# Kernel tuning notes

Measured on AMD Instinct MI355X. Metric: run time of the kernel, lower is better.

Reference implementation:

```python
import jax, jax.numpy as jnp
import numpy as np

EPS = 1e-8  # torch F.cosine_similarity eps


def setup_inputs() -> dict:
    key = jax.random.key(0)
    B, CAP, CD, CTX = 32, 32768, 64, 64
    ks = jax.random.split(key, 9)
    inp = {
        "query_content": jax.random.normal(ks[0], (B, CD), jnp.float32),
        "query_context": jax.random.normal(ks[1], (B, CTX), jnp.float32),
        "memory_content": 0.1 * jax.random.normal(ks[2], (CAP, CD), jnp.float32),
        "memory_contexts": 0.1 * jax.random.normal(ks[3], (CAP, CTX), jnp.float32),
        "memory_freshness": jnp.ones((CAP,), jnp.float32),
        "W1": jax.random.normal(ks[4], (2 * CD, CD), jnp.float32) / np.sqrt(2 * CD),
        "b1": 0.01 * jax.random.normal(ks[5], (CD,), jnp.float32),
        "W2": jax.random.normal(ks[6], (CD, 1), jnp.float32) / np.sqrt(CD),
        "b2": 0.01 * jax.random.normal(ks[7], (1,), jnp.float32),
        "top_k": 16,
    }
    return inp


def reference(query_content, query_context, memory_content, memory_contexts,
              memory_freshness, W1, b1, W2, b2, top_k):
    B, CD = query_content.shape
    # similarity_calculator MLP over all (query, memory) pairs.
    # Linear on concat([q, m]) == q @ W1[:CD] + m @ W1[CD:]  (avoids the concat).
    q_part = query_content @ W1[:CD]            # [B, CD]
    m_part = memory_content @ W1[CD:]           # [CAP, CD]
    h = jax.nn.relu(q_part[:, None, :] + m_part[None, :, :] + b1)  # [B, CAP, CD]
    content_sim = jax.nn.sigmoid(jnp.einsum('bch,h->bc', h, W2[:, 0]) + b2[0])  # [B, CAP]

    # cosine similarity between query_context and each stored context
    qn = query_context / jnp.maximum(jnp.linalg.norm(query_context, axis=-1, keepdims=True), EPS)
    mn = memory_contexts / jnp.maximum(jnp.linalg.norm(memory_contexts, axis=-1, keepdims=True), EPS)
    context_sim = qn @ mn.T                      # [B, CAP]

    time_weights = memory_freshness              # time_mask is all-ones in source
    final = 0.5 * content_sim + 0.3 * context_sim + 0.2 * time_weights[None, :]

    top_similarities, top_indices = jax.lax.top_k(final, top_k)   # [B, k]
    retrieved_content = memory_content[top_indices]               # [B, k, CD]
    retrieved_time_weights = time_weights[top_indices]            # [B, k]
    return (retrieved_content, top_similarities, retrieved_time_weights)
```

## Files before the change

kernel.cpp:

```cpp
#include <hip/hip_runtime.h>
#include <math.h>

#define CAP   32768
#define NB    32
#define ROWS  64
#define NBLK  (CAP / ROWS)
#define TOPK  16
#define CEPS  1e-8f

#define PITCH 68
#define CHUNK 2048
#define NCHUNK (CAP / CHUNK)

#define WS_QP    0
#define WS_QN    2048
#define WS_FINAL 4096

__global__ __launch_bounds__(64) void prep_kernel(
    const float* __restrict__ qc,
    const float* __restrict__ qctx,
    const float* __restrict__ W1,
    const float* __restrict__ b1,
    float* __restrict__ ws)
{
    const int b = blockIdx.x;
    const int j = threadIdx.x;

    float a0 = b1[j], a1 = 0.f, a2 = 0.f, a3 = 0.f;
    #pragma unroll
    for (int i = 0; i < 64; i += 4) {
        a0 = fmaf(qc[b * 64 + i + 0], W1[(i + 0) * 64 + j], a0);
        a1 = fmaf(qc[b * 64 + i + 1], W1[(i + 1) * 64 + j], a1);
        a2 = fmaf(qc[b * 64 + i + 2], W1[(i + 2) * 64 + j], a2);
        a3 = fmaf(qc[b * 64 + i + 3], W1[(i + 3) * 64 + j], a3);
    }
    ws[WS_QP + b * 64 + j] = (a0 + a1) + (a2 + a3);

    float x = qctx[b * 64 + j];
    float ss = x * x;
    ss += __shfl_xor(ss, 1,  64);
    ss += __shfl_xor(ss, 2,  64);
    ss += __shfl_xor(ss, 4,  64);
    ss += __shfl_xor(ss, 8,  64);
    ss += __shfl_xor(ss, 16, 64);
    ss += __shfl_xor(ss, 32, 64);
    ws[WS_QN + b * 64 + j] = x / fmaxf(sqrtf(ss), CEPS);
}

__global__ __launch_bounds__(256) void score_kernel(
    const float* __restrict__ mcont,
    const float* __restrict__ mctx,
    const float* __restrict__ fresh,
    const float* __restrict__ W1,
    const float* __restrict__ W2,
    const float* __restrict__ b2,
    float* __restrict__ ws)
{
    __shared__ float s_mc[ROWS * PITCH];
    __shared__ float s_qp[NB * PITCH];
    __shared__ float s_qn[NB * PITCH];
    __shared__ float s_base[ROWS];
    __shared__ float s_inv[ROWS];

    const int tid = threadIdx.x;
    const int C0 = blockIdx.x * ROWS;

    const float4* g_mc = (const float4*)(mcont + (size_t)C0 * 64);
    #pragma unroll
    for (int t = tid; t < ROWS * 16; t += 256) {
        int r = t >> 4, c4 = t & 15;
        *(float4*)&s_mc[r * PITCH + c4 * 4] = g_mc[t];
    }
    const float4* g_qp = (const float4*)(ws + WS_QP);
    const float4* g_qn = (const float4*)(ws + WS_QN);
    #pragma unroll
    for (int t = tid; t < NB * 16; t += 256) {
        int r = t >> 4, c4 = t & 15;
        *(float4*)&s_qp[r * PITCH + c4 * 4] = g_qp[t];
        *(float4*)&s_qn[r * PITCH + c4 * 4] = g_qn[t];
    }
    {
        const int r = tid >> 2, q = tid & 3;
        const float* xr = mctx + (size_t)(C0 + r) * 64 + q * 16;
        float ss = 0.f;
        #pragma unroll
        for (int i = 0; i < 4; ++i) {
            float4 x = *(const float4*)&xr[i * 4];
            ss = fmaf(x.x, x.x, ss); ss = fmaf(x.y, x.y, ss);
            ss = fmaf(x.z, x.z, ss); ss = fmaf(x.w, x.w, ss);
        }
        ss += __shfl_xor(ss, 1, 64);
        ss += __shfl_xor(ss, 2, 64);
        if (q == 0) {
            s_inv[r]  = 0.3f / fmaxf(sqrtf(ss), CEPS);
            s_base[r] = 0.2f * fresh[C0 + r];
        }
    }
    __syncthreads();

    const int c_lo = tid & 15;
    const int j0 = (tid >> 4) * 4;
    {
        float acc[4][4] = {{0.f}};
        #pragma unroll 4
        for (int i4 = 0; i4 < 16; ++i4) {
            float4 w0 = *(const float4*)&W1[(64 + i4 * 4 + 0) * 64 + j0];
            float4 w1r = *(const float4*)&W1[(64 + i4 * 4 + 1) * 64 + j0];
            float4 w2r = *(const float4*)&W1[(64 + i4 * 4 + 2) * 64 + j0];
            float4 w3r = *(const float4*)&W1[(64 + i4 * 4 + 3) * 64 + j0];
            #pragma unroll
            for (int ci = 0; ci < 4; ++ci) {
                float4 m = *(const float4*)&s_mc[(c_lo + 16 * ci) * PITCH + i4 * 4];
                acc[ci][0] = fmaf(m.x, w0.x, acc[ci][0]);
                acc[ci][1] = fmaf(m.x, w0.y, acc[ci][1]);
                acc[ci][2] = fmaf(m.x, w0.z, acc[ci][2]);
                acc[ci][3] = fmaf(m.x, w0.w, acc[ci][3]);
                acc[ci][0] = fmaf(m.y, w1r.x, acc[ci][0]);
                acc[ci][1] = fmaf(m.y, w1r.y, acc[ci][1]);
                acc[ci][2] = fmaf(m.y, w1r.z, acc[ci][2]);
                acc[ci][3] = fmaf(m.y, w1r.w, acc[ci][3]);
                acc[ci][0] = fmaf(m.z, w2r.x, acc[ci][0]);
                acc[ci][1] = fmaf(m.z, w2r.y, acc[ci][1]);
                acc[ci][2] = fmaf(m.z, w2r.z, acc[ci][2]);
                acc[ci][3] = fmaf(m.z, w2r.w, acc[ci][3]);
                acc[ci][0] = fmaf(m.w, w3r.x, acc[ci][0]);
                acc[ci][1] = fmaf(m.w, w3r.y, acc[ci][1]);
                acc[ci][2] = fmaf(m.w, w3r.z, acc[ci][2]);
                acc[ci][3] = fmaf(m.w, w3r.w, acc[ci][3]);
            }
        }
        __syncthreads();
        #pragma unroll
        for (int jj = 0; jj < 4; ++jj)
            #pragma unroll
            for (int ci = 0; ci < 4; ++ci)
                s_mc[(j0 + jj) * PITCH + c_lo + 16 * ci] = acc[ci][jj];
    }
    __syncthreads();

    const int bq = (tid & 15) << 1;
    const int cq = (tid >> 4) << 2;
    float4 a1v[2];
    a1v[0] = make_float4(0.f, 0.f, 0.f, 0.f);
    a1v[1] = make_float4(0.f, 0.f, 0.f, 0.f);
    float a2[2][4] = {{0.f}};
    const float* mxb = mctx + (size_t)C0 * 64;

    #pragma unroll 4
    for (int j4 = 0; j4 < 16; ++j4) {
        const int jo = j4 * 4;
        float4 w2v = *(const float4*)(W2 + jo);
        float4 qp0 = *(const float4*)&s_qp[ bq      * PITCH + jo];
        float4 qp1 = *(const float4*)&s_qp[(bq + 1) * PITCH + jo];
        float4 qn0 = *(const float4*)&s_qn[ bq      * PITCH + jo];
        float4 qn1 = *(const float4*)&s_qn[(bq + 1) * PITCH + jo];
        float4 m0 = *(const float4*)&s_mc[(jo + 0) * PITCH + cq];
        float4 m1 = *(const float4*)&s_mc[(jo + 1) * PITCH + cq];
        float4 m2 = *(const float4*)&s_mc[(jo + 2) * PITCH + cq];
        float4 m3 = *(const float4*)&s_mc[(jo + 3) * PITCH + cq];

        #pragma unroll
        for (int bi = 0; bi < 2; ++bi) {
            float4 qp = bi ? qp1 : qp0;
            float4& av = a1v[bi];
            av.x = fmaf(fmaxf(qp.x + m0.x, 0.f), w2v.x, av.x);
            av.y = fmaf(fmaxf(qp.x + m0.y, 0.f), w2v.x, av.y);
            av.z = fmaf(fmaxf(qp.x + m0.z, 0.f), w2v.x, av.z);
            av.w = fmaf(fmaxf(qp.x + m0.w, 0.f), w2v.x, av.w);
            av.x = fmaf(fmaxf(qp.y + m1.x, 0.f), w2v.y, av.x);
            av.y = fmaf(fmaxf(qp.y + m1.y, 0.f), w2v.y, av.y);
            av.z = fmaf(fmaxf(qp.y + m1.z, 0.f), w2v.y, av.z);
            av.w = fmaf(fmaxf(qp.y + m1.w, 0.f), w2v.y, av.w);
            av.x = fmaf(fmaxf(qp.z + m2.x, 0.f), w2v.z, av.x);
            av.y = fmaf(fmaxf(qp.z + m2.y, 0.f), w2v.z, av.y);
            av.z = fmaf(fmaxf(qp.z + m2.z, 0.f), w2v.z, av.z);
            av.w = fmaf(fmaxf(qp.z + m2.w, 0.f), w2v.z, av.w);
            av.x = fmaf(fmaxf(qp.w + m3.x, 0.f), w2v.w, av.x);
            av.y = fmaf(fmaxf(qp.w + m3.y, 0.f), w2v.w, av.y);
            av.z = fmaf(fmaxf(qp.w + m3.z, 0.f), w2v.w, av.z);
            av.w = fmaf(fmaxf(qp.w + m3.w, 0.f), w2v.w, av.w);
        }
        #pragma unroll
        for (int ci = 0; ci < 4; ++ci) {
            float4 xv = *(const float4*)&mxb[(cq + ci) * 64 + jo];
            a2[0][ci] = fmaf(qn0.x, xv.x, a2[0][ci]);
            a2[0][ci] = fmaf(qn0.y, xv.y, a2[0][ci]);
            a2[0][ci] = fmaf(qn0.z, xv.z, a2[0][ci]);
            a2[0][ci] = fmaf(qn0.w, xv.w, a2[0][ci]);
            a2[1][ci] = fmaf(qn1.x, xv.x, a2[1][ci]);
            a2[1][ci] = fmaf(qn1.y, xv.y, a2[1][ci]);
            a2[1][ci] = fmaf(qn1.z, xv.z, a2[1][ci]);
            a2[1][ci] = fmaf(qn1.w, xv.w, a2[1][ci]);
        }
    }

    const float b2v = b2[0];
    float4 inv4  = *(const float4*)&s_inv[cq];
    float4 base4 = *(const float4*)&s_base[cq];
    #pragma unroll
    for (int bi = 0; bi < 2; ++bi) {
        float4 r;
        r.x = 0.5f / (1.f + expf(-(a1v[bi].x + b2v))) + a2[bi][0] * inv4.x + base4.x;
        r.y = 0.5f / (1.f + expf(-(a1v[bi].y + b2v))) + a2[bi][1] * inv4.y + base4.y;
        r.z = 0.5f / (1.f + expf(-(a1v[bi].z + b2v))) + a2[bi][2] * inv4.z + base4.z;
        r.w = 0.5f / (1.f + expf(-(a1v[bi].w + b2v))) + a2[bi][3] * inv4.w + base4.w;
        *(float4*)&ws[WS_FINAL + (size_t)(bq + bi) * CAP + C0 + cq] = r;
    }
}

__device__ __forceinline__ void bitonic64_desc(float& v, int& iv, int lane)
{
    #pragma unroll
    for (int k = 2; k <= 64; k <<= 1) {
        #pragma unroll
        for (int j = k >> 1; j > 0; j >>= 1) {
            float ov = __shfl_xor(v, j, 64);
            int   oi = __shfl_xor(iv, j, 64);
            bool low        = (lane & j) == 0;
            bool dirDesc    = (lane & k) == 0;
            bool takeBetter = (low == dirDesc);
            bool otherBetter = (ov > v) || (ov == v && oi < iv);
            if (otherBetter == takeBetter) { v = ov; iv = oi; }
        }
    }
}

__global__ __launch_bounds__(256) void topk_stage1(float* __restrict__ ws)
{
    __shared__ float s_val[64];
    __shared__ int   s_idx[64];

    const int lane = threadIdx.x & 63;
    const int w    = threadIdx.x >> 6;
    const int b    = blockIdx.y;
    float* row = ws + WS_FINAL + (size_t)b * CAP;
    const int cbase = blockIdx.x * CHUNK;
    const int sb = cbase + w * 512;

    float v[8];
    #pragma unroll
    for (int g = 0; g < 2; ++g) {
        float4 t = *(const float4*)&row[sb + g * 256 + lane * 4];
        v[4 * g + 0] = t.x; v[4 * g + 1] = t.y;
        v[4 * g + 2] = t.z; v[4 * g + 3] = t.w;
    }

    float outv = 0.f;
    int   outi = 0;

    for (int k = 0; k < TOPK; ++k) {
        float bv = v[0]; int bj = 0;
        #pragma unroll
        for (int j = 1; j < 8; ++j)
            if (v[j] > bv) { bv = v[j]; bj = j; }
        int bi = sb + (bj >> 2) * 256 + lane * 4 + (bj & 3);

        #pragma unroll
        for (int off = 1; off < 64; off <<= 1) {
            float ov = __shfl_xor(bv, off, 64);
            int   oi = __shfl_xor(bi, off, 64);
            if (ov > bv || (ov == bv && oi < bi)) { bv = ov; bi = oi; }
        }
        if (lane == k) { outv = bv; outi = bi; }

        int rel = bi - sb;
        bool mine = (((rel >> 2) & 63) == lane);
        int wj = ((rel >> 8) << 2) | (rel & 3);
        #pragma unroll
        for (int j = 0; j < 8; ++j)
            if (mine && wj == j) v[j] = -INFINITY;
    }

    if (lane < TOPK) {
        s_val[w * TOPK + lane] = outv;
        s_idx[w * TOPK + lane] = outi;
    }
    __syncthreads();
    if (w != 0) return;

    float mv = s_val[lane];
    int   mi = s_idx[lane];
    bitonic64_desc(mv, mi, lane);
    if (lane < TOPK) {
        row[cbase + lane]        = mv;
        row[cbase + TOPK + lane] = __int_as_float(mi);
    }
}

__global__ __launch_bounds__(256) void topk_stage2(
    const float* __restrict__ mcont,
    const float* __restrict__ fresh,
    const float* __restrict__ ws,
    float* __restrict__ out)
{
    __shared__ float s_val[64];
    __shared__ int   s_idx[64];

    const int lane = threadIdx.x & 63;
    const int w    = threadIdx.x >> 6;
    const int b    = blockIdx.x;
    const float* row = ws + WS_FINAL + (size_t)b * CAP;

    const int ch  = w * 4 + (lane >> 4);
    const int pos = lane & 15;
    float mv = row[ch * CHUNK + pos];
    int   mi = __float_as_int(row[ch * CHUNK + TOPK + pos]);
    bitonic64_desc(mv, mi, lane);

    if (lane < TOPK) {
        s_val[w * TOPK + lane] = mv;
        s_idx[w * TOPK + lane] = mi;
    }
    __syncthreads();
    if (w != 0) return;

    float fv = s_val[lane];
    int   fi = s_idx[lane];
    bitonic64_desc(fv, fi, lane);

    float* out_content = out;
    float* out_sim     = out + NB * TOPK * 64;
    float* out_tw      = out + NB * TOPK * 64 + NB * TOPK;

    if (lane < TOPK) {
        out_sim[b * TOPK + lane] = fv;
        out_tw [b * TOPK + lane] = fresh[fi];
    }

    #pragma unroll
    for (int r = 0; r < TOPK; ++r) {
        int wi = __shfl(fi, r, 64);
        out_content[(size_t)b * TOPK * 64 + r * 64 + lane] =
            mcont[(size_t)wi * 64 + lane];
    }
}

extern "C" void kernel_launch(void* const* d_in, const int* in_sizes, int n_in,
                              void* d_out, int out_size, void* d_ws, size_t ws_size,
                              hipStream_t stream) {
    const float* qc    = (const float*)d_in[0];
    const float* qctx  = (const float*)d_in[1];
    const float* mcont = (const float*)d_in[2];
    const float* mctx  = (const float*)d_in[3];
    const float* fresh = (const float*)d_in[4];
    const float* W1    = (const float*)d_in[5];
    const float* b1    = (const float*)d_in[6];
    const float* W2    = (const float*)d_in[7];
    const float* b2    = (const float*)d_in[8];
    float* out = (float*)d_out;
    float* ws  = (float*)d_ws;

    prep_kernel<<<NB, 64, 0, stream>>>(qc, qctx, W1, b1, ws);
    score_kernel<<<NBLK, 256, 0, stream>>>(mcont, mctx, fresh, W1, W2, b2, ws);
    topk_stage1<<<dim3(NCHUNK, NB), 256, 0, stream>>>(ws);
    topk_stage2<<<NB, 256, 0, stream>>>(mcont, fresh, ws, out);
}
```

Measured before the change: 125.9 us.

## Replace iterative top-k extraction with bitonic sorts and halve chunk size

Stage-1 top-k previously ran 16 rounds of wave-wide argmax reductions over 8 values per lane. It now sorts four 64-element columns with bitonic networks and merges their top-16s with one more bitonic pass. The chunk size drops to 1024, which doubles the number of stage-1 blocks. Stage 2 grows to 512 threads with an extra merge level to absorb the 32 chunk candidate lists. This trades serial shuffle reductions for parallel sorting networks, at the cost of more blocks and more intermediate candidates.

Measured after the change: 125.9 us, median of 2. About the same (-0.0%).

```diff
diff --git a/kernel.cpp b/kernel.cpp
--- a/kernel.cpp
+++ b/kernel.cpp
@@ -9,7 +9,7 @@
 #define CEPS  1e-8f
 
 #define PITCH 68
-#define CHUNK 2048
+#define CHUNK 1024
 #define NCHUNK (CAP / CHUNK)
 
 #define WS_QP    0
@@ -235,45 +235,34 @@
     const int b    = blockIdx.y;
     float* row = ws + WS_FINAL + (size_t)b * CAP;
     const int cbase = blockIdx.x * CHUNK;
-    const int sb = cbase + w * 512;
-
-    float v[8];
-    #pragma unroll
-    for (int g = 0; g < 2; ++g) {
-        float4 t = *(const float4*)&row[sb + g * 256 + lane * 4];
-        v[4 * g + 0] = t.x; v[4 * g + 1] = t.y;
-        v[4 * g + 2] = t.z; v[4 * g + 3] = t.w;
-    }
-
-    float outv = 0.f;
-    int   outi = 0;
-
-    for (int k = 0; k < TOPK; ++k) {
-        float bv = v[0]; int bj = 0;
-        #pragma unroll
-        for (int j = 1; j < 8; ++j)
-            if (v[j] > bv) { bv = v[j]; bj = j; }
-        int bi = sb + (bj >> 2) * 256 + lane * 4 + (bj & 3);
-
-        #pragma unroll
-        for (int off = 1; off < 64; off <<= 1) {
-            float ov = __shfl_xor(bv, off, 64);
-            int   oi = __shfl_xor(bi, off, 64);
-            if (ov > bv || (ov == bv && oi < bi)) { bv = ov; bi = oi; }
-        }
-        if (lane == k) { outv = bv; outi = bi; }
-
-        int rel = bi - sb;
-        bool mine = (((rel >> 2) & 63) == lane);
-        int wj = ((rel >> 8) << 2) | (rel & 3);
-        #pragma unroll
-        for (int j = 0; j < 8; ++j)
-            if (mine && wj == j) v[j] = -INFINITY;
-    }
+    const int sb = cbase + w * 256;
+
+    float4 t = *(const float4*)&row[sb + lane * 4];
+    float v0 = t.x, v1 = t.y, v2 = t.z, v3 = t.w;
+    int   i0 = sb + lane * 4 + 0;
+    int   i1 = sb + lane * 4 + 1;
+    int   i2 = sb + lane * 4 + 2;
+    int   i3 = sb + lane * 4 + 3;
+
+    bitonic64_desc(v0, i0, lane);
+    bitonic64_desc(v1, i1, lane);
+    bitonic64_desc(v2, i2, lane);
+    bitonic64_desc(v3, i3, lane);
+
+    const int r = lane & 15;
+    float c0 = __shfl(v0, r, 64), c1 = __shfl(v1, r, 64);
+    float c2 = __shfl(v2, r, 64), c3 = __shfl(v3, r, 64);
+    int   d0 = __shfl(i0, r, 64), d1 = __shfl(i1, r, 64);
+    int   d2 = __shfl(i2, r, 64), d3 = __shfl(i3, r, 64);
+    const int s = lane >> 4;
+    float cv = (s == 0) ? c0 : (s == 1) ? c1 : (s == 2) ? c2 : c3;
+    int   ci = (s == 0) ? d0 : (s == 1) ? d1 : (s == 2) ? d2 : d3;
+
+    bitonic64_desc(cv, ci, lane);
 
     if (lane < TOPK) {
-        s_val[w * TOPK + lane] = outv;
-        s_idx[w * TOPK + lane] = outi;
+        s_val[w * TOPK + lane] = cv;
+        s_idx[w * TOPK + lane] = ci;
     }
     __syncthreads();
     if (w != 0) return;
@@ -287,35 +276,49 @@
     }
 }
 
-__global__ __launch_bounds__(256) void topk_stage2(
+__global__ __launch_bounds__(512) void topk_stage2(
     const float* __restrict__ mcont,
     const float* __restrict__ fresh,
     const float* __restrict__ ws,
     float* __restrict__ out)
 {
-    __shared__ float s_val[64];
-    __shared__ int   s_idx[64];
+    __shared__ float s_v1[128];
+    __shared__ int   s_i1[128];
+    __shared__ float s_v2[32];
+    __shared__ int   s_i2[32];
 
     const int lane = threadIdx.x & 63;
     const int w    = threadIdx.x >> 6;
     const int b    = blockIdx.x;
     const float* row = ws + WS_FINAL + (size_t)b * CAP;
 
-    const int ch  = w * 4 + (lane >> 4);
-    const int pos = lane & 15;
-    float mv = row[ch * CHUNK + pos];
-    int   mi = __float_as_int(row[ch * CHUNK + TOPK + pos]);
-    bitonic64_desc(mv, mi, lane);
-
-    if (lane < TOPK) {
-        s_val[w * TOPK + lane] = mv;
-        s_idx[w * TOPK + lane] = mi;
+    {
+        const int cand = w * 64 + lane;
+        const int ch = cand >> 4, pos = cand & 15;
+        float v  = row[ch * CHUNK + pos];
+        int   iv = __float_as_int(row[ch * CHUNK + TOPK + pos]);
+        bitonic64_desc(v, iv, lane);
+        if (lane < TOPK) {
+            s_v1[w * TOPK + lane] = v;
+            s_i1[w * TOPK + lane] = iv;
+        }
+    }
+    __syncthreads();
+
+    if (w < 2) {
+        float v  = s_v1[w * 64 + lane];
+        int   iv = s_i1[w * 64 + lane];
+        bitonic64_desc(v, iv, lane);
+        if (lane < TOPK) {
+            s_v2[w * TOPK + lane] = v;
+            s_i2[w * TOPK + lane] = iv;
+        }
     }
     __syncthreads();
     if (w != 0) return;
 
-    float fv = s_val[lane];
-    int   fi = s_idx[lane];
+    float fv = (lane < 32) ? s_v2[lane] : -INFINITY;
+    int   fi = (lane < 32) ? s_i2[lane] : 0x7FFFFFFF;
     bitonic64_desc(fv, fi, lane);
 
     float* out_content = out;
@@ -353,5 +356,5 @@
     prep_kernel<<<NB, 64, 0, stream>>>(qc, qctx, W1, b1, ws);
     score_kernel<<<NBLK, 256, 0, stream>>>(mcont, mctx, fresh, W1, W2, b2, ws);
     topk_stage1<<<dim3(NCHUNK, NB), 256, 0, stream>>>(ws);
-    topk_stage2<<<NB, 256, 0, stream>>>(mcont, fresh, ws, out);
-}
+    topk_stage2<<<NB, 512, 0, stream>>>(mcont, fresh, ws, out);
+}
```
